# Kernel tuning notes

Hardware: AMD Instinct MI355X
Metric: run time of the kernel (lower is better)

## Reference

```python
import jax, jax.numpy as jnp
import numpy as np

N = 50000    # nodes
E = 640000   # edges (avg degree ~12.8)
D = 128      # feature dim (input = hidden = output)
L = 3        # num_layers
BN_EPS = 1e-5


def setup_inputs() -> dict:
    key = jax.random.key(0)
    ks = jax.random.split(key, 6)
    x = jax.random.normal(ks[0], (N, D), dtype=jnp.float32)
    edge_index = jax.random.randint(ks[1], (2, E), 0, N, dtype=jnp.int32)
    s = 1.0 / np.sqrt(D)
    # Weights stored as (in, out); equivalent to torch Linear's x @ W.T with W:(out,in).
    W1 = jax.random.normal(ks[2], (L, D, D), dtype=jnp.float32) * s
    b1 = jnp.zeros((L, D), dtype=jnp.float32)
    gamma = jnp.ones((L, D), dtype=jnp.float32)   # BatchNorm weight
    beta = jnp.zeros((L, D), dtype=jnp.float32)   # BatchNorm bias
    W2 = jax.random.normal(ks[3], (L, D, D), dtype=jnp.float32) * s
    b2 = jnp.zeros((L, D), dtype=jnp.float32)
    return {"x": x, "W1": W1, "b1": b1, "gamma": gamma, "beta": beta,
            "W2": W2, "b2": b2, "edge_index": edge_index}


def reference(x, W1, b1, gamma, beta, W2, b2, edge_index):
    src = edge_index[0]
    dst = edge_index[1]
    h = x
    for i in range(L):
        # GINConv aggregation: sum of source-node features into destinations, eps=0
        agg = jax.ops.segment_sum(h[src], dst, num_segments=N)   # [N, D]
        z = h + agg                                              # (1+eps)*x + sum_j x_j
        # MLP: Linear -> BatchNorm1d (training stats) -> ReLU -> Linear
        z = z @ W1[i] + b1[i]
        mu = jnp.mean(z, axis=0)
        var = jnp.mean((z - mu) ** 2, axis=0)                    # biased var (torch BN)
        z = (z - mu) * jax.lax.rsqrt(var + BN_EPS) * gamma[i] + beta[i]
        z = jax.nn.relu(z)
        z = z @ W2[i] + b2[i]
        # inter-layer ReLU (dropout_rate=0 -> identity)
        h = jax.nn.relu(z) if i < L - 1 else z
    return h
```

## Files before the change

### kernel.cpp

```cpp
#include <hip/hip_runtime.h>

#define D 128
#define BN_EPS 1e-5f
#define ELLW 64
#define SGRP 8

typedef __bf16 bf16_t;
typedef __bf16 bf16x8 __attribute__((ext_vector_type(8)));
typedef __bf16 bf16x4 __attribute__((ext_vector_type(4)));
typedef __bf16 bf16x2 __attribute__((ext_vector_type(2)));
typedef float floatx4 __attribute__((ext_vector_type(4)));

__global__ void prep(const float* __restrict__ x, bf16_t* __restrict__ hb,
                     const float* __restrict__ W1, const float* __restrict__ W2,
                     bf16_t* __restrict__ Wsw, int* __restrict__ deg,
                     float* __restrict__ stats, int N, int n4) {
  int i = blockIdx.x * blockDim.x + threadIdx.x;
  if (i < n4) {
    float4 v = ((const float4*)x)[i];
    bf16x4 p;
    p[0] = (bf16_t)v.x; p[1] = (bf16_t)v.y; p[2] = (bf16_t)v.z; p[3] = (bf16_t)v.w;
    *(bf16x4*)(hb + (size_t)4 * i) = p;
  }
  if (i < N) deg[i] = 0;
  if (i < 3 * SGRP * 256) stats[i] = 0.f;
  if (i < 6 * 16384) {
    int mat = i >> 14;
    int kn = i & 16383;
    int k = kn >> 7;
    int n = kn & 127;
    const float* Wm = (mat < 3) ? (W1 + (size_t)mat * 16384)
                                : (W2 + (size_t)(mat - 3) * 16384);
    float v = Wm[kn];
    int f = ((n >> 4) << 2) | (k >> 5);
    int ln = (((k >> 3) & 3) << 4) | (n & 15);
    int j = k & 7;
    Wsw[(size_t)mat * 16384 + ((f << 6) + ln) * 8 + j] = (bf16_t)v;
  }
}

__global__ void ell_fill(const int* __restrict__ src, const int* __restrict__ dst,
                         int* __restrict__ deg, int* __restrict__ ell, int E) {
  int e = blockIdx.x * blockDim.x + threadIdx.x;
  if (e < E) {
    int d = dst[e];
    int slot = atomicAdd(&deg[d], 1);
    if (slot < ELLW) ell[(size_t)d * ELLW + slot] = src[e];
  }
}

__global__ __launch_bounds__(256) void agg_gemm1(
    const bf16_t* __restrict__ h, bf16_t* __restrict__ z,
    const int* __restrict__ ell, const int* __restrict__ deg,
    const bf16_t* __restrict__ Wsw1, const float* __restrict__ bias1,
    float* __restrict__ stats, int N) {
  __shared__ bf16_t T[64][136];
  __shared__ float sred[256];
  const int t = threadIdx.x;
  const int wv = t >> 6;
  const int lane = t & 63;
  const int half = lane >> 5;
  const int s = lane & 31;
  const int off = s << 2;
  const int l15 = lane & 15;
  const int quad = lane >> 4;
  const int rowBaseBlk = blockIdx.x * 64;

  sred[t] = 0.f;

  for (int p = 0; p < 8; ++p) {
    const int lrow = wv * 16 + (p << 1) + half;
    const int node = rowBaseBlk + lrow;
    floatx4 A0 = {0.f, 0.f, 0.f, 0.f};
    floatx4 A1 = {0.f, 0.f, 0.f, 0.f};
    floatx4 A2 = {0.f, 0.f, 0.f, 0.f};
    floatx4 A3 = {0.f, 0.f, 0.f, 0.f};
    if (node < N) {
      int dg = deg[node]; if (dg > ELLW) dg = ELLW;
      const int* nb = ell + (size_t)node * ELLW;
      bf16x4 sv = *(const bf16x4*)(h + (size_t)node * D + off);
      A0[0] = (float)sv[0]; A0[1] = (float)sv[1];
      A0[2] = (float)sv[2]; A0[3] = (float)sv[3];
      int e = 0;
      for (; e + 8 <= dg; e += 8) {
        int4 ia = *(const int4*)(nb + e);
        int4 ib = *(const int4*)(nb + e + 4);
        bf16x4 v0 = *(const bf16x4*)(h + (size_t)ia.x * D + off);
        bf16x4 v1 = *(const bf16x4*)(h + (size_t)ia.y * D + off);
        bf16x4 v2 = *(const bf16x4*)(h + (size_t)ia.z * D + off);
        bf16x4 v3 = *(const bf16x4*)(h + (size_t)ia.w * D + off);
        bf16x4 v4 = *(const bf16x4*)(h + (size_t)ib.x * D + off);
        bf16x4 v5 = *(const bf16x4*)(h + (size_t)ib.y * D + off);
        bf16x4 v6 = *(const bf16x4*)(h + (size_t)ib.z * D + off);
        bf16x4 v7 = *(const bf16x4*)(h + (size_t)ib.w * D + off);
#pragma unroll
        for (int j = 0; j < 4; ++j) {
          A0[j] += (float)v0[j];
          A1[j] += (float)v1[j];
          A2[j] += (float)v2[j];
          A3[j] += (float)v3[j];
          A0[j] += (float)v4[j];
          A1[j] += (float)v5[j];
          A2[j] += (float)v6[j];
          A3[j] += (float)v7[j];
        }
      }
      for (; e + 4 <= dg; e += 4) {
        int4 i4 = *(const int4*)(nb + e);
        bf16x4 v0 = *(const bf16x4*)(h + (size_t)i4.x * D + off);
        bf16x4 v1 = *(const bf16x4*)(h + (size_t)i4.y * D + off);
        bf16x4 v2 = *(const bf16x4*)(h + (size_t)i4.z * D + off);
        bf16x4 v3 = *(const bf16x4*)(h + (size_t)i4.w * D + off);
#pragma unroll
        for (int j = 0; j < 4; ++j) {
          A0[j] += (float)v0[j];
          A1[j] += (float)v1[j];
          A2[j] += (float)v2[j];
          A3[j] += (float)v3[j];
        }
      }
      for (; e < dg; ++e) {
        bf16x4 v = *(const bf16x4*)(h + (size_t)nb[e] * D + off);
#pragma unroll
        for (int j = 0; j < 4; ++j) A0[j] += (float)v[j];
      }
    }
#pragma unroll
    for (int j = 0; j < 4; ++j) A0[j] += A1[j] + A2[j] + A3[j];
    bf16x4 o;
    o[0] = (bf16_t)A0[0]; o[1] = (bf16_t)A0[1];
    o[2] = (bf16_t)A0[2]; o[3] = (bf16_t)A0[3];
    *(bf16x4*)&T[lrow][off] = o;
    if (node < N) *(bf16x4*)(z + (size_t)node * D + off) = o;
  }
  __syncthreads();

  bf16x8 a[4];
#pragma unroll
  for (int kc = 0; kc < 4; ++kc)
    a[kc] = *(const bf16x8*)&T[wv * 16 + l15][kc * 32 + quad * 8];

  floatx4 acc[8];
#pragma unroll
  for (int nt = 0; nt < 8; ++nt) {
    float bv = bias1[nt * 16 + l15];
    acc[nt] = (floatx4){bv, bv, bv, bv};
  }
#pragma unroll
  for (int nt = 0; nt < 8; ++nt) {
#pragma unroll
    for (int kc = 0; kc < 4; ++kc) {
      bf16x8 b = *(const bf16x8*)(Wsw1 + (size_t)((nt * 4 + kc) * 64 + lane) * 8);
      acc[nt] = __builtin_amdgcn_mfma_f32_16x16x32_bf16(a[kc], b, acc[nt], 0, 0, 0);
    }
  }

  const int rowBase = rowBaseBlk + wv * 16 + quad * 4;
#pragma unroll
  for (int nt = 0; nt < 8; ++nt) {
    int c = nt * 16 + l15;
    float sum = 0.f, q = 0.f;
#pragma unroll
    for (int r = 0; r < 4; ++r) {
      if (rowBase + r < N) {
        float v = acc[nt][r];
        sum += v; q += v * v;
      }
    }
    sum += __shfl_xor(sum, 16); sum += __shfl_xor(sum, 32);
    q += __shfl_xor(q, 16); q += __shfl_xor(q, 32);
    if (quad == 0) {
      atomicAdd(&sred[c], sum);
      atomicAdd(&sred[128 + c], q);
    }
  }
  __syncthreads();
  atomicAdd(&stats[((blockIdx.x & (SGRP - 1)) << 8) + t], sred[t]);
}

__global__ __launch_bounds__(256) void mlp2r(
    const bf16_t* __restrict__ Z, const float* __restrict__ stats,
    const float* __restrict__ gamma, const float* __restrict__ beta,
    const bf16_t* __restrict__ Wsw1, const float* __restrict__ bias1,
    const bf16_t* __restrict__ Wsw2, const float* __restrict__ bias2,
    void* __restrict__ outp, int nStrips, int N, float invN,
    int relu_out, int fp32_out) {
  __shared__ bf16_t T[64][136];
  __shared__ float abL[256];
  const int t = threadIdx.x;
  const int wv = t >> 6;
  const int lane = t & 63;
  const int l15 = lane & 15;
  const int quad = lane >> 4;
  const int strip = blockIdx.x * 4 + wv;
  const bool active = strip < nStrips;

  if (t < 128) {
    float s0 = 0.f, q0 = 0.f;
#pragma unroll
    for (int g = 0; g < SGRP; ++g) {
      s0 += stats[(g << 8) + t];
      q0 += stats[(g << 8) + 128 + t];
    }
    float mu = s0 * invN;
    float var = fmaxf(q0 * invN - mu * mu, 0.f);
    float ai = gamma[t] * rsqrtf(var + BN_EPS);
    abL[t] = ai;
    abL[128 + t] = beta[t] - mu * ai;
  }

  bf16x8 a[4];
  const int row = strip * 16 + l15;
  if (active && row < N) {
#pragma unroll
    for (int kc = 0; kc < 4; ++kc)
      a[kc] = *(const bf16x8*)(Z + (size_t)row * D + kc * 32 + quad * 8);
  } else {
#pragma unroll
    for (int kc = 0; kc < 4; ++kc)
#pragma unroll
      for (int j = 0; j < 8; ++j) a[kc][j] = (bf16_t)0.f;
  }

  floatx4 acc[8];
#pragma unroll
  for (int nt = 0; nt < 8; ++nt) {
    float bv = bias1[nt * 16 + l15];
    acc[nt] = (floatx4){bv, bv, bv, bv};
  }
#pragma unroll
  for (int nt = 0; nt < 8; ++nt) {
#pragma unroll
    for (int kc = 0; kc < 4; ++kc) {
      bf16x8 b = *(const bf16x8*)(Wsw1 + (size_t)((nt * 4 + kc) * 64 + lane) * 8);
      acc[nt] = __builtin_amdgcn_mfma_f32_16x16x32_bf16(a[kc], b, acc[nt], 0, 0, 0);
    }
  }

  __syncthreads();

  float bnA[8], bnB[8];
#pragma unroll
  for (int nt = 0; nt < 8; ++nt) {
    int c = nt * 16 + l15;
    bnA[nt] = abL[c];
    bnB[nt] = abL[128 + c];
  }

  const int lr = wv * 16 + quad * 4;
#pragma unroll
  for (int nt = 0; nt < 8; ++nt) {
    int c = nt * 16 + l15;
#pragma unroll
    for (int r = 0; r < 4; ++r)
      T[lr + r][c] = (bf16_t)fmaxf(fmaf(acc[nt][r], bnA[nt], bnB[nt]), 0.f);
  }
  __syncthreads();

  bf16x8 a2[4];
#pragma unroll
  for (int kc = 0; kc < 4; ++kc)
    a2[kc] = *(const bf16x8*)&T[wv * 16 + l15][kc * 32 + quad * 8];

#pragma unroll
  for (int nt = 0; nt < 8; ++nt) {
    float bv = bias2[nt * 16 + l15];
    acc[nt] = (floatx4){bv, bv, bv, bv};
  }
#pragma unroll
  for (int nt = 0; nt < 8; ++nt) {
#pragma unroll
    for (int kc = 0; kc < 4; ++kc) {
      bf16x8 b = *(const bf16x8*)(Wsw2 + (size_t)((nt * 4 + kc) * 64 + lane) * 8);
      acc[nt] = __builtin_amdgcn_mfma_f32_16x16x32_bf16(a2[kc], b, acc[nt], 0, 0, 0);
    }
  }

  if (!active) return;
  const int rowBase = strip * 16 + quad * 4;
  if (fp32_out) {
    float* out = (float*)outp;
#pragma unroll
    for (int nt = 0; nt < 8; ++nt) {
      int c = nt * 16 + l15;
#pragma unroll
      for (int r = 0; r < 4; ++r) {
        int rw = rowBase + r;
        if (rw < N) {
          float v = acc[nt][r];
          if (relu_out) v = fmaxf(v, 0.f);
          out[(size_t)rw * D + c] = v;
        }
      }
    }
  } else {
    bf16_t* out = (bf16_t*)outp;
#pragma unroll
    for (int nt = 0; nt < 8; ++nt) {
      int c = nt * 16 + l15;
#pragma unroll
      for (int r = 0; r < 4; ++r) {
        int rw = rowBase + r;
        if (rw < N) {
          float v = acc[nt][r];
          if (relu_out) v = fmaxf(v, 0.f);
          out[(size_t)rw * D + c] = (bf16_t)v;
        }
      }
    }
  }
}

extern "C" void kernel_launch(void* const* d_in, const int* in_sizes, int n_in,
                              void* d_out, int out_size, void* d_ws, size_t ws_size,
                              hipStream_t stream) {
  const float* x     = (const float*)d_in[0];
  const float* W1    = (const float*)d_in[1];
  const float* b1    = (const float*)d_in[2];
  const float* gamma = (const float*)d_in[3];
  const float* beta  = (const float*)d_in[4];
  const float* W2    = (const float*)d_in[5];
  const float* b2    = (const float*)d_in[6];
  const int*   ei    = (const int*)d_in[7];

  const int N = in_sizes[0] / D;
  const int E = in_sizes[7] / 2;
  const int* src = ei;
  const int* dst = ei + E;

  char* ws = (char*)d_ws;
  size_t bufBytes = (size_t)N * D * sizeof(bf16_t);
  bf16_t* hb   = (bf16_t*)ws;
  bf16_t* zb   = (bf16_t*)(ws + bufBytes);
  int*    ell  = (int*)(ws + 2 * bufBytes);
  int*    deg  = (int*)((char*)ell + (size_t)N * ELLW * sizeof(int));
  float*  stats = (float*)((char*)deg + (size_t)N * sizeof(int));
  bf16_t* Wsw  = (bf16_t*)(stats + 3 * SGRP * 256);

  const int n4 = N * D / 4;
  const int prepBlocks = (n4 + 255) / 256;
  const int eb = (E + 255) / 256;
  const int fusedBlocks = (N + 63) / 64;
  const int nStrips = (N + 15) / 16;
  const int gemmBlocks = (nStrips + 3) / 4;
  const float invN = 1.f / (float)N;

  prep<<<prepBlocks, 256, 0, stream>>>(x, hb, W1, W2, Wsw, deg, stats, N, n4);
  ell_fill<<<eb, 256, 0, stream>>>(src, dst, deg, ell, E);

  for (int i = 0; i < 3; ++i) {
    float* st = stats + (size_t)i * SGRP * 256;
    agg_gemm1<<<fusedBlocks, 256, 0, stream>>>(
        hb, zb, ell, deg, Wsw + (size_t)i * 16384, b1 + (size_t)i * D, st, N);
    void* Ob = (i == 2) ? d_out : (void*)hb;
    mlp2r<<<gemmBlocks, 256, 0, stream>>>(
        zb, st, gamma + (size_t)i * D, beta + (size_t)i * D,
        Wsw + (size_t)i * 16384, b1 + (size_t)i * D,
        Wsw + (size_t)(i + 3) * 16384, b2 + (size_t)i * D,
        Ob, nStrips, N, invN, (i < 2) ? 1 : 0, (i == 2) ? 1 : 0);
  }
}
```

Measured before the change: 309.7 us.

## Apply W1 before aggregation and fuse next-layer W1 into second MLP kernel

Uses linearity, (h+Ah)W1 = hW1 + A(hW1), to apply the first linear layer before the neighbour gather. Aggregation becomes a standalone gather-plus-BN-stats kernel, and the second MLP kernel now also applies the next layer's W1, so the first GEMM is no longer recomputed twice per layer. This removes the duplicated W1 GEMM and the shared-memory staging in the aggregation kernel. In exchange it adds one W1 GEMM launch at the start and one more workspace buffer, and rounding changes because the aggregation now sums bf16 products.

```diff
diff --git a/kernel.cpp b/kernel.cpp
--- a/kernel.cpp
+++ b/kernel.cpp
@@ -8,7 +8,6 @@
 typedef __bf16 bf16_t;
 typedef __bf16 bf16x8 __attribute__((ext_vector_type(8)));
 typedef __bf16 bf16x4 __attribute__((ext_vector_type(4)));
-typedef __bf16 bf16x2 __attribute__((ext_vector_type(2)));
 typedef float floatx4 __attribute__((ext_vector_type(4)));
 
 __global__ void prep(const float* __restrict__ x, bf16_t* __restrict__ hb,
@@ -49,103 +48,33 @@
   }
 }
 
-__global__ __launch_bounds__(256) void agg_gemm1(
-    const bf16_t* __restrict__ h, bf16_t* __restrict__ z,
-    const int* __restrict__ ell, const int* __restrict__ deg,
-    const bf16_t* __restrict__ Wsw1, const float* __restrict__ bias1,
-    float* __restrict__ stats, int N) {
-  __shared__ bf16_t T[64][136];
-  __shared__ float sred[256];
+__global__ __launch_bounds__(256) void gemmW1(
+    const bf16_t* __restrict__ H, const bf16_t* __restrict__ Wsw1,
+    bf16_t* __restrict__ G, int nStrips, int N) {
   const int t = threadIdx.x;
   const int wv = t >> 6;
   const int lane = t & 63;
-  const int half = lane >> 5;
-  const int s = lane & 31;
-  const int off = s << 2;
   const int l15 = lane & 15;
   const int quad = lane >> 4;
-  const int rowBaseBlk = blockIdx.x * 64;
-
-  sred[t] = 0.f;
-
-  for (int p = 0; p < 8; ++p) {
-    const int lrow = wv * 16 + (p << 1) + half;
-    const int node = rowBaseBlk + lrow;
-    floatx4 A0 = {0.f, 0.f, 0.f, 0.f};
-    floatx4 A1 = {0.f, 0.f, 0.f, 0.f};
-    floatx4 A2 = {0.f, 0.f, 0.f, 0.f};
-    floatx4 A3 = {0.f, 0.f, 0.f, 0.f};
-    if (node < N) {
-      int dg = deg[node]; if (dg > ELLW) dg = ELLW;
-      const int* nb = ell + (size_t)node * ELLW;
-      bf16x4 sv = *(const bf16x4*)(h + (size_t)node * D + off);
-      A0[0] = (float)sv[0]; A0[1] = (float)sv[1];
-      A0[2] = (float)sv[2]; A0[3] = (float)sv[3];
-      int e = 0;
-      for (; e + 8 <= dg; e += 8) {
-        int4 ia = *(const int4*)(nb + e);
-        int4 ib = *(const int4*)(nb + e + 4);
-        bf16x4 v0 = *(const bf16x4*)(h + (size_t)ia.x * D + off);
-        bf16x4 v1 = *(const bf16x4*)(h + (size_t)ia.y * D + off);
-        bf16x4 v2 = *(const bf16x4*)(h + (size_t)ia.z * D + off);
-        bf16x4 v3 = *(const bf16x4*)(h + (size_t)ia.w * D + off);
-        bf16x4 v4 = *(const bf16x4*)(h + (size_t)ib.x * D + off);
-        bf16x4 v5 = *(const bf16x4*)(h + (size_t)ib.y * D + off);
-        bf16x4 v6 = *(const bf16x4*)(h + (size_t)ib.z * D + off);
-        bf16x4 v7 = *(const bf16x4*)(h + (size_t)ib.w * D + off);
-#pragma unroll
-        for (int j = 0; j < 4; ++j) {
-          A0[j] += (float)v0[j];
-          A1[j] += (float)v1[j];
-          A2[j] += (float)v2[j];
-          A3[j] += (float)v3[j];
-          A0[j] += (float)v4[j];
-          A1[j] += (float)v5[j];
-          A2[j] += (float)v6[j];
-          A3[j] += (float)v7[j];
-        }
-      }
-      for (; e + 4 <= dg; e += 4) {
-        int4 i4 = *(const int4*)(nb + e);
-        bf16x4 v0 = *(const bf16x4*)(h + (size_t)i4.x * D + off);
-        bf16x4 v1 = *(const bf16x4*)(h + (size_t)i4.y * D + off);
-        bf16x4 v2 = *(const bf16x4*)(h + (size_t)i4.z * D + off);
-        bf16x4 v3 = *(const bf16x4*)(h + (size_t)i4.w * D + off);
-#pragma unroll
-        for (int j = 0; j < 4; ++j) {
-          A0[j] += (float)v0[j];
-          A1[j] += (float)v1[j];
-          A2[j] += (float)v2[j];
-          A3[j] += (float)v3[j];
-        }
-      }
-      for (; e < dg; ++e) {
-        bf16x4 v = *(const bf16x4*)(h + (size_t)nb[e] * D + off);
-#pragma unroll
-        for (int j = 0; j < 4; ++j) A0[j] += (float)v[j];
-      }
-    }
-#pragma unroll
-    for (int j = 0; j < 4; ++j) A0[j] += A1[j] + A2[j] + A3[j];
-    bf16x4 o;
-    o[0] = (bf16_t)A0[0]; o[1] = (bf16_t)A0[1];
-    o[2] = (bf16_t)A0[2]; o[3] = (bf16_t)A0[3];
-    *(bf16x4*)&T[lrow][off] = o;
-    if (node < N) *(bf16x4*)(z + (size_t)node * D + off) = o;
-  }
-  __syncthreads();
+  const int strip = blockIdx.x * 4 + wv;
+  if (strip >= nStrips) return;
 
   bf16x8 a[4];
-#pragma unroll
-  for (int kc = 0; kc < 4; ++kc)
-    a[kc] = *(const bf16x8*)&T[wv * 16 + l15][kc * 32 + quad * 8];
+  const int row = strip * 16 + l15;
+  if (row < N) {
+#pragma unroll
+    for (int kc = 0; kc < 4; ++kc)
+      a[kc] = *(const bf16x8*)(H + (size_t)row * D + kc * 32 + quad * 8);
+  } else {
+#pragma unroll
+    for (int kc = 0; kc < 4; ++kc)
+#pragma unroll
+      for (int j = 0; j < 8; ++j) a[kc][j] = (bf16_t)0.f;
+  }
 
   floatx4 acc[8];
 #pragma unroll
-  for (int nt = 0; nt < 8; ++nt) {
-    float bv = bias1[nt * 16 + l15];
-    acc[nt] = (floatx4){bv, bv, bv, bv};
-  }
+  for (int nt = 0; nt < 8; ++nt) acc[nt] = (floatx4){0.f, 0.f, 0.f, 0.f};
 #pragma unroll
   for (int nt = 0; nt < 8; ++nt) {
 #pragma unroll
@@ -155,36 +84,122 @@
     }
   }
 
-  const int rowBase = rowBaseBlk + wv * 16 + quad * 4;
+  const int rowBase = strip * 16 + quad * 4;
 #pragma unroll
   for (int nt = 0; nt < 8; ++nt) {
     int c = nt * 16 + l15;
-    float sum = 0.f, q = 0.f;
 #pragma unroll
     for (int r = 0; r < 4; ++r) {
-      if (rowBase + r < N) {
-        float v = acc[nt][r];
-        sum += v; q += v * v;
+      int rw = rowBase + r;
+      if (rw < N) G[(size_t)rw * D + c] = (bf16_t)acc[nt][r];
+    }
+  }
+}
+
+__global__ __launch_bounds__(256) void agg_stats(
+    const bf16_t* __restrict__ G, bf16_t* __restrict__ Y,
+    const int* __restrict__ ell, const int* __restrict__ deg,
+    const float* __restrict__ bias1, float* __restrict__ stats, int Nn) {
+  __shared__ float sred[256];
+  const int t = threadIdx.x;
+  sred[t] = 0.f;
+
+  const int node = blockIdx.x * 8 + (t >> 5);
+  const int s = t & 31;
+  const int off = s << 2;
+  const bool valid = node < Nn;
+
+  floatx4 A0 = {0.f, 0.f, 0.f, 0.f};
+  floatx4 A1 = {0.f, 0.f, 0.f, 0.f};
+  floatx4 A2 = {0.f, 0.f, 0.f, 0.f};
+  floatx4 A3 = {0.f, 0.f, 0.f, 0.f};
+  if (valid) {
+    int dg = deg[node]; if (dg > ELLW) dg = ELLW;
+    const int* nb = ell + (size_t)node * ELLW;
+    float4 bv = *(const float4*)(bias1 + off);
+    bf16x4 sv = *(const bf16x4*)(G + (size_t)node * D + off);
+    A0[0] = bv.x + (float)sv[0]; A0[1] = bv.y + (float)sv[1];
+    A0[2] = bv.z + (float)sv[2]; A0[3] = bv.w + (float)sv[3];
+    int e = 0;
+    for (; e + 8 <= dg; e += 8) {
+      int4 ia = *(const int4*)(nb + e);
+      int4 ib = *(const int4*)(nb + e + 4);
+      bf16x4 v0 = *(const bf16x4*)(G + (size_t)ia.x * D + off);
+      bf16x4 v1 = *(const bf16x4*)(G + (size_t)ia.y * D + off);
+      bf16x4 v2 = *(const bf16x4*)(G + (size_t)ia.z * D + off);
+      bf16x4 v3 = *(const bf16x4*)(G + (size_t)ia.w * D + off);
+      bf16x4 v4 = *(const bf16x4*)(G + (size_t)ib.x * D + off);
+      bf16x4 v5 = *(const bf16x4*)(G + (size_t)ib.y * D + off);
+      bf16x4 v6 = *(const bf16x4*)(G + (size_t)ib.z * D + off);
+      bf16x4 v7 = *(const bf16x4*)(G + (size_t)ib.w * D + off);
+#pragma unroll
+      for (int j = 0; j < 4; ++j) {
+        A0[j] += (float)v0[j];
+        A1[j] += (float)v1[j];
+        A2[j] += (float)v2[j];
+        A3[j] += (float)v3[j];
+        A0[j] += (float)v4[j];
+        A1[j] += (float)v5[j];
+        A2[j] += (float)v6[j];
+        A3[j] += (float)v7[j];
       }
     }
-    sum += __shfl_xor(sum, 16); sum += __shfl_xor(sum, 32);
-    q += __shfl_xor(q, 16); q += __shfl_xor(q, 32);
-    if (quad == 0) {
-      atomicAdd(&sred[c], sum);
-      atomicAdd(&sred[128 + c], q);
+    for (; e + 4 <= dg; e += 4) {
+      int4 i4 = *(const int4*)(nb + e);
+      bf16x4 v0 = *(const bf16x4*)(G + (size_t)i4.x * D + off);
+      bf16x4 v1 = *(const bf16x4*)(G + (size_t)i4.y * D + off);
+      bf16x4 v2 = *(const bf16x4*)(G + (size_t)i4.z * D + off);
+      bf16x4 v3 = *(const bf16x4*)(G + (size_t)i4.w * D + off);
+#pragma unroll
+      for (int j = 0; j < 4; ++j) {
+        A0[j] += (float)v0[j];
+        A1[j] += (float)v1[j];
+        A2[j] += (float)v2[j];
+        A3[j] += (float)v3[j];
+      }
+    }
+    for (; e < dg; ++e) {
+      bf16x4 v = *(const bf16x4*)(G + (size_t)nb[e] * D + off);
+#pragma unroll
+      for (int j = 0; j < 4; ++j) A0[j] += (float)v[j];
+    }
+  }
+#pragma unroll
+  for (int j = 0; j < 4; ++j) A0[j] += A1[j] + A2[j] + A3[j];
+
+  bf16x4 o;
+  o[0] = (bf16_t)A0[0]; o[1] = (bf16_t)A0[1];
+  o[2] = (bf16_t)A0[2]; o[3] = (bf16_t)A0[3];
+  if (valid) *(bf16x4*)(Y + (size_t)node * D + off) = o;
+
+  float s4[4], q4[4];
+#pragma unroll
+  for (int j = 0; j < 4; ++j) {
+    float v = valid ? (float)o[j] : 0.f;
+    s4[j] = v; q4[j] = v * v;
+  }
+#pragma unroll
+  for (int j = 0; j < 4; ++j) {
+    s4[j] += __shfl_xor(s4[j], 32);
+    q4[j] += __shfl_xor(q4[j], 32);
+  }
+  if ((t & 63) < 32) {
+#pragma unroll
+    for (int j = 0; j < 4; ++j) {
+      atomicAdd(&sred[off + j], s4[j]);
+      atomicAdd(&sred[128 + off + j], q4[j]);
     }
   }
   __syncthreads();
   atomicAdd(&stats[((blockIdx.x & (SGRP - 1)) << 8) + t], sred[t]);
 }
 
-__global__ __launch_bounds__(256) void mlp2r(
-    const bf16_t* __restrict__ Z, const float* __restrict__ stats,
+__global__ __launch_bounds__(256) void mlp2g(
+    const bf16_t* __restrict__ Y, const float* __restrict__ stats,
     const float* __restrict__ gamma, const float* __restrict__ beta,
-    const bf16_t* __restrict__ Wsw1, const float* __restrict__ bias1,
     const bf16_t* __restrict__ Wsw2, const float* __restrict__ bias2,
-    void* __restrict__ outp, int nStrips, int N, float invN,
-    int relu_out, int fp32_out) {
+    const bf16_t* __restrict__ Wsw1n, void* __restrict__ outp,
+    int nStrips, int N, float invN, int last) {
   __shared__ bf16_t T[64][136];
   __shared__ float abL[256];
   const int t = threadIdx.x;
@@ -209,59 +224,33 @@
     abL[128 + t] = beta[t] - mu * ai;
   }
 
-  bf16x8 a[4];
+  bf16x8 ay[4];
   const int row = strip * 16 + l15;
   if (active && row < N) {
 #pragma unroll
     for (int kc = 0; kc < 4; ++kc)
-      a[kc] = *(const bf16x8*)(Z + (size_t)row * D + kc * 32 + quad * 8);
+      ay[kc] = *(const bf16x8*)(Y + (size_t)row * D + kc * 32 + quad * 8);
   } else {
 #pragma unroll
     for (int kc = 0; kc < 4; ++kc)
 #pragma unroll
-      for (int j = 0; j < 8; ++j) a[kc][j] = (bf16_t)0.f;
+      for (int j = 0; j < 8; ++j) ay[kc][j] = (bf16_t)0.f;
+  }
+
+  __syncthreads();
+
+  bf16x8 a2[4];
+#pragma unroll
+  for (int kc = 0; kc < 4; ++kc) {
+#pragma unroll
+    for (int j = 0; j < 8; ++j) {
+      int c = kc * 32 + quad * 8 + j;
+      float v = fmaxf(fmaf((float)ay[kc][j], abL[c], abL[128 + c]), 0.f);
+      a2[kc][j] = (bf16_t)v;
+    }
   }
 
   floatx4 acc[8];
-#pragma unroll
-  for (int nt = 0; nt < 8; ++nt) {
-    float bv = bias1[nt * 16 + l15];
-    acc[nt] = (floatx4){bv, bv, bv, bv};
-  }
-#pragma unroll
-  for (int nt = 0; nt < 8; ++nt) {
-#pragma unroll
-    for (int kc = 0; kc < 4; ++kc) {
-      bf16x8 b = *(const bf16x8*)(Wsw1 + (size_t)((nt * 4 + kc) * 64 + lane) * 8);
-      acc[nt] = __builtin_amdgcn_mfma_f32_16x16x32_bf16(a[kc], b, acc[nt], 0, 0, 0);
-    }
-  }
-
-  __syncthreads();
-
-  float bnA[8], bnB[8];
-#pragma unroll
-  for (int nt = 0; nt < 8; ++nt) {
-    int c = nt * 16 + l15;
-    bnA[nt] = abL[c];
-    bnB[nt] = abL[128 + c];
-  }
-
-  const int lr = wv * 16 + quad * 4;
-#pragma unroll
-  for (int nt = 0; nt < 8; ++nt) {
-    int c = nt * 16 + l15;
-#pragma unroll
-    for (int r = 0; r < 4; ++r)
-      T[lr + r][c] = (bf16_t)fmaxf(fmaf(acc[nt][r], bnA[nt], bnB[nt]), 0.f);
-  }
-  __syncthreads();
-
-  bf16x8 a2[4];
-#pragma unroll
-  for (int kc = 0; kc < 4; ++kc)
-    a2[kc] = *(const bf16x8*)&T[wv * 16 + l15][kc * 32 + quad * 8];
-
 #pragma unroll
   for (int nt = 0; nt < 8; ++nt) {
     float bv = bias2[nt * 16 + l15];
@@ -276,9 +265,9 @@
     }
   }
 
-  if (!active) return;
   const int rowBase = strip * 16 + quad * 4;
-  if (fp32_out) {
+  if (last) {
+    if (!active) return;
     float* out = (float*)outp;
 #pragma unroll
     for (int nt = 0; nt < 8; ++nt) {
@@ -286,27 +275,47 @@
 #pragma unroll
       for (int r = 0; r < 4; ++r) {
         int rw = rowBase + r;
-        if (rw < N) {
-          float v = acc[nt][r];
-          if (relu_out) v = fmaxf(v, 0.f);
-          out[(size_t)rw * D + c] = v;
-        }
+        if (rw < N) out[(size_t)rw * D + c] = acc[nt][r];
       }
     }
-  } else {
-    bf16_t* out = (bf16_t*)outp;
-#pragma unroll
-    for (int nt = 0; nt < 8; ++nt) {
-      int c = nt * 16 + l15;
-#pragma unroll
-      for (int r = 0; r < 4; ++r) {
-        int rw = rowBase + r;
-        if (rw < N) {
-          float v = acc[nt][r];
-          if (relu_out) v = fmaxf(v, 0.f);
-          out[(size_t)rw * D + c] = (bf16_t)v;
-        }
-      }
+    return;
+  }
+
+  const int lr = wv * 16 + quad * 4;
+#pragma unroll
+  for (int nt = 0; nt < 8; ++nt) {
+    int c = nt * 16 + l15;
+#pragma unroll
+    for (int r = 0; r < 4; ++r)
+      T[lr + r][c] = (bf16_t)fmaxf(acc[nt][r], 0.f);
+  }
+  __syncthreads();
+
+  bf16x8 ah[4];
+#pragma unroll
+  for (int kc = 0; kc < 4; ++kc)
+    ah[kc] = *(const bf16x8*)&T[wv * 16 + l15][kc * 32 + quad * 8];
+
+#pragma unroll
+  for (int nt = 0; nt < 8; ++nt) acc[nt] = (floatx4){0.f, 0.f, 0.f, 0.f};
+#pragma unroll
+  for (int nt = 0; nt < 8; ++nt) {
+#pragma unroll
+    for (int kc = 0; kc < 4; ++kc) {
+      bf16x8 b = *(const bf16x8*)(Wsw1n + (size_t)((nt * 4 + kc) * 64 + lane) * 8);
+      acc[nt] = __builtin_amdgcn_mfma_f32_16x16x32_bf16(ah[kc], b, acc[nt], 0, 0, 0);
+    }
+  }
+
+  if (!active) return;
+  bf16_t* Gout = (bf16_t*)outp;
+#pragma unroll
+  for (int nt = 0; nt < 8; ++nt) {
+    int c = nt * 16 + l15;
+#pragma unroll
+    for (int r = 0; r < 4; ++r) {
+      int rw = rowBase + r;
+      if (rw < N) Gout[(size_t)rw * D + c] = (bf16_t)acc[nt][r];
     }
   }
 }
@@ -331,8 +340,9 @@
   char* ws = (char*)d_ws;
   size_t bufBytes = (size_t)N * D * sizeof(bf16_t);
   bf16_t* hb   = (bf16_t*)ws;
-  bf16_t* zb   = (bf16_t*)(ws + bufBytes);
-  int*    ell  = (int*)(ws + 2 * bufBytes);
+  bf16_t* Gb   = (bf16_t*)(ws + bufBytes);
+  bf16_t* Yb   = (bf16_t*)(ws + 2 * bufBytes);
+  int*    ell  = (int*)(ws + 3 * bufBytes);
   int*    deg  = (int*)((char*)ell + (size_t)N * ELLW * sizeof(int));
   float*  stats = (float*)((char*)deg + (size_t)N * sizeof(int));
   bf16_t* Wsw  = (bf16_t*)(stats + 3 * SGRP * 256);
@@ -340,23 +350,24 @@
   const int n4 = N * D / 4;
   const int prepBlocks = (n4 + 255) / 256;
   const int eb = (E + 255) / 256;
-  const int fusedBlocks = (N + 63) / 64;
+  const int aggBlocks = (N + 7) / 8;
   const int nStrips = (N + 15) / 16;
   const int gemmBlocks = (nStrips + 3) / 4;
   const float invN = 1.f / (float)N;
 
   prep<<<prepBlocks, 256, 0, stream>>>(x, hb, W1, W2, Wsw, deg, stats, N, n4);
   ell_fill<<<eb, 256, 0, stream>>>(src, dst, deg, ell, E);
+  gemmW1<<<gemmBlocks, 256, 0, stream>>>(hb, Wsw, Gb, nStrips, N);
 
   for (int i = 0; i < 3; ++i) {
     float* st = stats + (size_t)i * SGRP * 256;
-    agg_gemm1<<<fusedBlocks, 256, 0, stream>>>(
-        hb, zb, ell, deg, Wsw + (size_t)i * 16384, b1 + (size_t)i * D, st, N);
-    void* Ob = (i == 2) ? d_out : (void*)hb;
-    mlp2r<<<gemmBlocks, 256, 0, stream>>>(
-        zb, st, gamma + (size_t)i * D, beta + (size_t)i * D,
-        Wsw + (size_t)i * 16384, b1 + (size_t)i * D,
+    agg_stats<<<aggBlocks, 256, 0, stream>>>(
+        Gb, Yb, ell, deg, b1 + (size_t)i * D, st, N);
+    void* Ob = (i == 2) ? d_out : (void*)Gb;
+    mlp2g<<<gemmBlocks, 256, 0, stream>>>(
+        Yb, st, gamma + (size_t)i * D, beta + (size_t)i * D,
         Wsw + (size_t)(i + 3) * 16384, b2 + (size_t)i * D,
-        Ob, nStrips, N, invN, (i < 2) ? 1 : 0, (i == 2) ? 1 : 0);
-  }
-}
+        Wsw + (size_t)(i + 1 < 3 ? i + 1 : 0) * 16384,
+        Ob, nStrips, N, invN, (i == 2) ? 1 : 0);
+  }
+}
```

Result: slower. 339.3 us (+9.5%).
